# Optimization experiments

Measured on AMD Instinct MI355X. Metric: run time of the kernel, lower is better.

Reference implementation:

```python
import jax, jax.numpy as jnp
import numpy as np

N_NODES = 50000
N_EDGES = 400000
IN_DIM = 8
HIDDEN = 768
N_LAYERS = 4
LN_EPS = 1e-5


def setup_inputs() -> dict:
    key = jax.random.key(0)
    ks = jax.random.split(key, 10)
    x = jax.random.normal(ks[0], (N_NODES, IN_DIM), dtype=jnp.float32)
    edge_index = jax.random.randint(ks[1], (2, N_EDGES), 0, N_NODES, dtype=jnp.int32)
    # input projection
    s_in = 1.0 / np.sqrt(IN_DIM)
    Wp = jax.random.uniform(ks[2], (HIDDEN, IN_DIM), jnp.float32, -s_in, s_in)
    bp = jax.random.uniform(ks[3], (HIDDEN,), jnp.float32, -s_in, s_in)
    # stacked per-layer SAGEConv params (all layers have out_c == HIDDEN here)
    s_h = 1.0 / np.sqrt(HIDDEN)
    Wl = jax.random.uniform(ks[4], (N_LAYERS, HIDDEN, HIDDEN), jnp.float32, -s_h, s_h)  # lin_l (aggregated neighbors), has bias
    bl = jax.random.uniform(ks[5], (N_LAYERS, HIDDEN), jnp.float32, -s_h, s_h)
    Wr = jax.random.uniform(ks[6], (N_LAYERS, HIDDEN, HIDDEN), jnp.float32, -s_h, s_h)  # lin_r (root), no bias
    # LayerNorm params
    gamma = jnp.ones((N_LAYERS, HIDDEN), dtype=jnp.float32)
    beta = jnp.zeros((N_LAYERS, HIDDEN), dtype=jnp.float32)
    return {"x": x, "Wp": Wp, "bp": bp, "Wl": Wl, "bl": bl, "Wr": Wr,
            "gamma": gamma, "beta": beta, "edge_index": edge_index}


def _layer_norm(h, g, b):
    mu = jnp.mean(h, axis=-1, keepdims=True)
    var = jnp.mean(jnp.square(h - mu), axis=-1, keepdims=True)
    return (h - mu) * jax.lax.rsqrt(var + LN_EPS) * g + b


def reference(x, Wp, bp, Wl, bl, Wr, gamma, beta, edge_index):
    n = x.shape[0]
    src, dst = edge_index[0], edge_index[1]
    # in-degree per target node, clamped for mean
    deg = jax.ops.segment_sum(jnp.ones_like(dst, dtype=x.dtype), dst, num_segments=n)
    inv_deg = 1.0 / jnp.maximum(deg, 1.0)

    h = x @ Wp.T + bp  # [N, HIDDEN]

    def layer(h, params):
        Wl_i, bl_i, Wr_i, g_i, b_i = params
        # mean aggregation of source features at targets: [N, C]
        agg = jax.ops.segment_sum(h[src], dst, num_segments=n) * inv_deg[:, None]
        out = agg @ Wl_i.T + bl_i + h @ Wr_i.T  # SAGEConv
        out = _layer_norm(jax.nn.silu(out), g_i, b_i)  # norm(silu(conv))
        return out, None

    h, _ = jax.lax.scan(layer, h, (Wl, bl, Wr, gamma, beta))
    return h
```

## Files before the change

### kernel.cpp

```cpp
#include <hip/hip_runtime.h>

#define NN 50000
#define NE 400000
#define HID 768
#define NL 4

typedef short bf16x8_t __attribute__((ext_vector_type(8)));
typedef float f32x4_t __attribute__((ext_vector_type(4)));

__device__ __forceinline__ unsigned short f2bf(float f) {
  union { float f; unsigned int u; } c; c.f = f;
  unsigned int u = c.u;
  u += 0x7FFF + ((u >> 16) & 1);
  return (unsigned short)(u >> 16);
}
__device__ __forceinline__ float bf2f(unsigned short s) {
  union { unsigned int u; float f; } c; c.u = ((unsigned int)s) << 16;
  return c.f;
}

__device__ __forceinline__ void async16(const void* g, void* l) {
  __builtin_amdgcn_global_load_lds((const __attribute__((address_space(1))) void*)g,
                                   (__attribute__((address_space(3))) void*)l,
                                   16, 0, 0);
}

__global__ void k_zero2(int* __restrict__ a, int* __restrict__ b, int n) {
  int i = blockIdx.x * blockDim.x + threadIdx.x;
  if (i < n) { a[i] = 0; b[i] = 0; }
}

__global__ void k_cvt(const float* __restrict__ a, unsigned short* __restrict__ o, int n) {
  int i = blockIdx.x * blockDim.x + threadIdx.x;
  if (i < n) o[i] = f2bf(a[i]);
}

__global__ __launch_bounds__(256) void k_inproj(const float* __restrict__ x,
                                                const float* __restrict__ Wp,
                                                const float* __restrict__ bp,
                                                unsigned short* __restrict__ h) {
  int n = blockIdx.x;
  __shared__ float xs[8];
  if (threadIdx.x < 8) xs[threadIdx.x] = x[n * 8 + threadIdx.x];
  __syncthreads();
  for (int j = threadIdx.x; j < HID; j += 256) {
    const float* w = Wp + j * 8;
    float s = bp[j];
#pragma unroll
    for (int k = 0; k < 8; ++k) s += xs[k] * w[k];
    h[(size_t)n * HID + j] = f2bf(s);
  }
}

__global__ void k_deg(const int* __restrict__ dst, int* __restrict__ deg) {
  int i = blockIdx.x * blockDim.x + threadIdx.x;
  if (i < NE) atomicAdd(&deg[dst[i]], 1);
}

__global__ __launch_bounds__(1024) void k_scan(const int* __restrict__ deg, int* __restrict__ rowptr) {
  __shared__ int sm[1024];
  const int chunk = 49;
  int t = threadIdx.x;
  int start = t * chunk;
  int end = min(start + chunk, NN);
  int local = 0;
  for (int i = start; i < end; ++i) local += deg[i];
  sm[t] = local;
  __syncthreads();
  for (int off = 1; off < 1024; off <<= 1) {
    int v = (t >= off) ? sm[t - off] : 0;
    __syncthreads();
    sm[t] += v;
    __syncthreads();
  }
  int run = sm[t] - local;
  for (int i = start; i < end; ++i) { rowptr[i] = run; run += deg[i]; }
  if (start < NN && end == NN) rowptr[NN] = run;
}

__global__ void k_fill(const int* __restrict__ src, const int* __restrict__ dst,
                       const int* __restrict__ rowptr, int* __restrict__ cursor,
                       int* __restrict__ csr) {
  int i = blockIdx.x * blockDim.x + threadIdx.x;
  if (i < NE) {
    int d = dst[i];
    int pos = atomicAdd(&cursor[d], 1);
    csr[rowptr[d] + pos] = src[i];
  }
}

__global__ __launch_bounds__(192) void k_agg(const unsigned short* __restrict__ h,
                                             const int* __restrict__ csr,
                                             const int* __restrict__ rowptr,
                                             unsigned short* __restrict__ agg) {
  int n = blockIdx.x;
  int t = threadIdx.x;
  int beg = rowptr[n], end = rowptr[n + 1];
  float a0 = 0.f, a1 = 0.f, a2 = 0.f, a3 = 0.f;
  for (int i = beg; i < end; ++i) {
    int s = csr[i];
    ushort4 v = *(const ushort4*)(h + (size_t)s * HID + t * 4);
    a0 += bf2f(v.x); a1 += bf2f(v.y); a2 += bf2f(v.z); a3 += bf2f(v.w);
  }
  float inv = 1.0f / (float)max(end - beg, 1);
  ushort4 o;
  o.x = f2bf(a0 * inv); o.y = f2bf(a1 * inv); o.z = f2bf(a2 * inv); o.w = f2bf(a3 * inv);
  *(ushort4*)(agg + (size_t)n * HID + t * 4) = o;
}

#define BM 256
#define BN 256
#define NKT 48
#define GGRID 588

__global__ __launch_bounds__(512, 2) void k_gemm(const unsigned short* __restrict__ A0,
                                                 const unsigned short* __restrict__ A1,
                                                 const unsigned short* __restrict__ B0,
                                                 const unsigned short* __restrict__ B1,
                                                 const float* __restrict__ bias,
                                                 unsigned short* __restrict__ sact, int M) {
  __shared__ __align__(16) unsigned short As[4][BM * 32];
  __shared__ __align__(16) unsigned short Bs[4][BN * 32];

  int b = blockIdx.x;
  int xcd = b & 7;
  int j = b >> 3;
  int o = xcd * 73 + min(xcd, 4) + j;
  int band = o / 3;
  int nt3 = o - band * 3;
  int m0 = band * BM;
  int n0 = nt3 * BN;

  int tid = threadIdx.x;
  int lane = tid & 63;
  int w = tid >> 6;
  int wm = w >> 2, wn = w & 3;

  int rl = tid >> 2;
  int kgs = (tid & 3) ^ ((rl >> 1) & 3);
  size_t aO = (size_t)(m0 + rl) * HID + kgs * 8;
  size_t bO = (size_t)(n0 + rl) * HID + kgs * 8;
  const size_t hstep = (size_t)128 * HID;

  auto stageA = [&](int t) {
    const unsigned short* A = (t < 24) ? A0 : A1;
    size_t kk = (size_t)(t - ((t < 24) ? 0 : 24)) * 32;
    int s = t & 3;
    async16(A + aO + kk,         &As[s][w * 512]);
    async16(A + aO + hstep + kk, &As[s][4096 + w * 512]);
  };
  auto stageB = [&](int t) {
    const unsigned short* B = (t < 24) ? B0 : B1;
    size_t kk = (size_t)(t - ((t < 24) ? 0 : 24)) * 32;
    int s = t & 3;
    async16(B + bO + kk,         &Bs[s][w * 512]);
    async16(B + bO + hstep + kk, &Bs[s][4096 + w * 512]);
  };

  int mr = lane & 15, kq = lane >> 4;
  int sq = (kq ^ ((mr >> 1) & 3)) * 8;

  f32x4_t acc[8][4] = {};

  stageA(0); stageB(0); stageA(1); stageB(1); stageA(2);
  asm volatile("s_waitcnt vmcnt(6)" ::: "memory");
  __builtin_amdgcn_s_barrier();

  for (int t = 0; t < NKT; ++t) {
    int s = t & 3;
    bf16x8_t af[4], ag[4], bf[4];
#pragma unroll
    for (int i = 0; i < 4; ++i)
      af[i] = *(const bf16x8_t*)&As[s][(wm * 128 + i * 16 + mr) * 32 + sq];
#pragma unroll
    for (int i = 0; i < 4; ++i)
      bf[i] = *(const bf16x8_t*)&Bs[s][(wn * 64 + i * 16 + mr) * 32 + sq];
    if (t <= 45) stageB(t + 2);
    __builtin_amdgcn_s_barrier();
    asm volatile("s_waitcnt lgkmcnt(0)" ::: "memory");
    __builtin_amdgcn_sched_barrier(0);
    __builtin_amdgcn_s_setprio(1);
#pragma unroll
    for (int mt = 0; mt < 4; ++mt)
#pragma unroll
      for (int nt = 0; nt < 4; ++nt)
        acc[mt][nt] = __builtin_amdgcn_mfma_f32_16x16x32_bf16(af[mt], bf[nt], acc[mt][nt], 0, 0, 0);
    __builtin_amdgcn_s_setprio(0);
    __builtin_amdgcn_s_barrier();
#pragma unroll
    for (int i = 0; i < 4; ++i)
      ag[i] = *(const bf16x8_t*)&As[s][(wm * 128 + (i + 4) * 16 + mr) * 32 + sq];
    if (t <= 44) stageA(t + 3);
    __builtin_amdgcn_s_barrier();
    asm volatile("s_waitcnt lgkmcnt(0)" ::: "memory");
    __builtin_amdgcn_sched_barrier(0);
    __builtin_amdgcn_s_setprio(1);
#pragma unroll
    for (int mt = 0; mt < 4; ++mt)
#pragma unroll
      for (int nt = 0; nt < 4; ++nt)
        acc[mt + 4][nt] = __builtin_amdgcn_mfma_f32_16x16x32_bf16(ag[mt], bf[nt], acc[mt + 4][nt], 0, 0, 0);
    __builtin_amdgcn_s_setprio(0);
    if (t <= 44)      asm volatile("s_waitcnt vmcnt(6)" ::: "memory");
    else if (t == 45) asm volatile("s_waitcnt vmcnt(4)" ::: "memory");
    else if (t == 46) asm volatile("s_waitcnt vmcnt(0)" ::: "memory");
    __builtin_amdgcn_s_barrier();
  }

  int col = lane & 15;
  int rq = (lane >> 4) * 4;
#pragma unroll
  for (int mt = 0; mt < 8; ++mt) {
#pragma unroll
    for (int nt = 0; nt < 4; ++nt) {
      int jj = n0 + wn * 64 + nt * 16 + col;
      float bv = bias[jj];
#pragma unroll
      for (int r = 0; r < 4; ++r) {
        int gm = m0 + wm * 128 + mt * 16 + rq + r;
        if (gm < M) {
          float v = acc[mt][nt][r] + bv;
          float sv = v / (1.f + __expf(-v));
          sact[(size_t)gm * HID + jj] = f2bf(sv);
        }
      }
    }
  }
}

__global__ __launch_bounds__(256) void k_ln(const unsigned short* __restrict__ sact,
                                            const float* __restrict__ gamma,
                                            const float* __restrict__ beta,
                                            unsigned short* __restrict__ hout,
                                            float* __restrict__ fout) {
  int n = blockIdx.x;
  const unsigned short* p = sact + (size_t)n * HID;
  float v[3];
  float sum = 0.f, sq = 0.f;
#pragma unroll
  for (int i = 0; i < 3; ++i) {
    float s = bf2f(p[threadIdx.x + i * 256]);
    v[i] = s; sum += s; sq += s * s;
  }
#pragma unroll
  for (int off = 32; off >= 1; off >>= 1) {
    sum += __shfl_down(sum, off);
    sq  += __shfl_down(sq, off);
  }
  __shared__ float rs[4], rq2[4];
  int wv = threadIdx.x >> 6;
  if ((threadIdx.x & 63) == 0) { rs[wv] = sum; rq2[wv] = sq; }
  __syncthreads();
  if (threadIdx.x == 0) {
    float s = rs[0] + rs[1] + rs[2] + rs[3];
    float q = rq2[0] + rq2[1] + rq2[2] + rq2[3];
    rs[0] = s / (float)HID;
    rq2[0] = q / (float)HID;
  }
  __syncthreads();
  float mu = rs[0];
  float var = rq2[0] - mu * mu;
  float inv = rsqrtf(var + 1e-5f);
#pragma unroll
  for (int i = 0; i < 3; ++i) {
    int j = threadIdx.x + i * 256;
    float y = (v[i] - mu) * inv * gamma[j] + beta[j];
    if (fout) fout[(size_t)n * HID + j] = y;
    else      hout[(size_t)n * HID + j] = f2bf(y);
  }
}

extern "C" void kernel_launch(void* const* d_in, const int* in_sizes, int n_in,
                              void* d_out, int out_size, void* d_ws, size_t ws_size,
                              hipStream_t stream) {
  const float* x     = (const float*)d_in[0];
  const float* Wp    = (const float*)d_in[1];
  const float* bp    = (const float*)d_in[2];
  const float* Wl    = (const float*)d_in[3];
  const float* bl    = (const float*)d_in[4];
  const float* Wr    = (const float*)d_in[5];
  const float* gamma = (const float*)d_in[6];
  const float* beta  = (const float*)d_in[7];
  const int*   ei    = (const int*)d_in[8];
  float* out = (float*)d_out;

  const int* src = ei;
  const int* dst = ei + NE;

  char* p = (char*)d_ws;
  unsigned short* h    = (unsigned short*)p;              p += (size_t)NN * HID * 2;
  unsigned short* agg  = (unsigned short*)p;              p += (size_t)NN * HID * 2;
  unsigned short* sact = (unsigned short*)p;              p += (size_t)NN * HID * 2;
  unsigned short* Wlb  = (unsigned short*)p;              p += (size_t)NL * HID * HID * 2;
  unsigned short* Wrb  = (unsigned short*)p;              p += (size_t)NL * HID * HID * 2;
  int* deg             = (int*)p;                         p += (size_t)NN * 4;
  int* rowptr          = (int*)p;                         p += (size_t)(NN + 1) * 4 + 12;
  int* cursor          = (int*)p;                         p += (size_t)NN * 4;
  int* csr             = (int*)p;                         p += (size_t)NE * 4;

  k_zero2<<<(NN + 255) / 256, 256, 0, stream>>>(deg, cursor, NN);
  int wn = NL * HID * HID;
  k_cvt<<<(wn + 255) / 256, 256, 0, stream>>>(Wl, Wlb, wn);
  k_cvt<<<(wn + 255) / 256, 256, 0, stream>>>(Wr, Wrb, wn);
  k_inproj<<<NN, 256, 0, stream>>>(x, Wp, bp, h);
  k_deg<<<(NE + 255) / 256, 256, 0, stream>>>(dst, deg);
  k_scan<<<1, 1024, 0, stream>>>(deg, rowptr);
  k_fill<<<(NE + 255) / 256, 256, 0, stream>>>(src, dst, rowptr, cursor, csr);

  for (int l = 0; l < NL; ++l) {
    k_agg<<<NN, 192, 0, stream>>>(h, csr, rowptr, agg);
    k_gemm<<<GGRID, 512, 0, stream>>>(agg, h,
                                      Wlb + (size_t)l * HID * HID,
                                      Wrb + (size_t)l * HID * HID,
                                      bl + (size_t)l * HID, sact, NN);
    k_ln<<<NN, 256, 0, stream>>>(sact, gamma + (size_t)l * HID, beta + (size_t)l * HID,
                                 h, (l == NL - 1) ? out : nullptr);
  }
}
```

Before: 1.742 ms.

## Load A fragments directly to registers and halve GEMM N-tile to 128

The GEMM drops the LDS staging of the A operand. Each wave now loads its A fragments straight from global memory into registers through a three-deep register pipeline, while B is still staged asynchronously in LDS. The N tile shrinks from 256 to 128, which doubles the grid and remaps blocks to XCDs over six column tiles. The aim is to cut LDS traffic and barriers and to raise parallelism, at the cost of more register pressure, A rows re-read from global/L2 by every wave, and less reuse of each tile.

```diff
diff --git a/kernel.cpp b/kernel.cpp
--- a/kernel.cpp
+++ b/kernel.cpp
@@ -109,9 +109,9 @@
 }
 
 #define BM 256
-#define BN 256
+#define BN 128
 #define NKT 48
-#define GGRID 588
+#define GGRID 1176
 
 __global__ __launch_bounds__(512, 2) void k_gemm(const unsigned short* __restrict__ A0,
                                                  const unsigned short* __restrict__ A1,
@@ -119,109 +119,101 @@
                                                  const unsigned short* __restrict__ B1,
                                                  const float* __restrict__ bias,
                                                  unsigned short* __restrict__ sact, int M) {
-  __shared__ __align__(16) unsigned short As[4][BM * 32];
   __shared__ __align__(16) unsigned short Bs[4][BN * 32];
 
   int b = blockIdx.x;
-  int xcd = b & 7;
-  int j = b >> 3;
-  int o = xcd * 73 + min(xcd, 4) + j;
-  int band = o / 3;
-  int nt3 = o - band * 3;
-  int m0 = band * BM;
-  int n0 = nt3 * BN;
-
-  int tid = threadIdx.x;
-  int lane = tid & 63;
-  int w = tid >> 6;
+  int xcd = b & 7, jj = b >> 3;
+  int o = xcd * 147 + jj;
+  int band = o / 6, nt6 = o % 6;
+  int m0 = band * BM, n0 = nt6 * BN;
+
+  int tid = threadIdx.x, lane = tid & 63, w = tid >> 6;
   int wm = w >> 2, wn = w & 3;
 
   int rl = tid >> 2;
   int kgs = (tid & 3) ^ ((rl >> 1) & 3);
-  size_t aO = (size_t)(m0 + rl) * HID + kgs * 8;
-  size_t bO = (size_t)(n0 + rl) * HID + kgs * 8;
-  const size_t hstep = (size_t)128 * HID;
-
-  auto stageA = [&](int t) {
-    const unsigned short* A = (t < 24) ? A0 : A1;
-    size_t kk = (size_t)(t - ((t < 24) ? 0 : 24)) * 32;
+  size_t bsrc = (size_t)(n0 + rl) * (HID * 2) + kgs * 16;
+
+  int mr = lane & 15, kq = lane >> 4;
+  unsigned voffA[8];
+#pragma unroll
+  for (int i = 0; i < 8; ++i)
+    voffA[i] = (unsigned)(((wm * 128 + i * 16 + mr) * HID + kq * 8) * 2);
+
+  int sq = (kq ^ ((mr >> 1) & 3)) * 8;
+  int boffe[2];
+#pragma unroll
+  for (int nt = 0; nt < 2; ++nt)
+    boffe[nt] = (wn * 32 + nt * 16 + mr) * 32 + sq;
+
+  const char* Abase0 = (const char*)A0 + (size_t)m0 * (HID * 2);
+  const char* Abase1 = (const char*)A1 + (size_t)m0 * (HID * 2);
+
+  f32x4_t acc[8][2] = {};
+  bf16x8_t aS0[8], aS1[8], aS2[8];
+
+  auto loadA = [&](int tt, bf16x8_t (&af)[8]) {
+    const char* Ab = (tt < 24 ? Abase0 : Abase1) + (size_t)(tt < 24 ? tt : tt - 24) * 64;
+#pragma unroll
+    for (int i = 0; i < 8; ++i) af[i] = *(const bf16x8_t*)(Ab + voffA[i]);
+  };
+  auto stageB = [&](int tt) {
+    const char* Bb = (const char*)(tt < 24 ? B0 : B1) + (size_t)(tt < 24 ? tt : tt - 24) * 64;
+    async16(Bb + bsrc, &Bs[tt & 3][w * 512]);
+  };
+
+  auto body = [&](int t, bf16x8_t (&af)[8], int W) {
+    if (W == 18)      asm volatile("s_waitcnt vmcnt(18)" ::: "memory");
+    else if (W == 9)  asm volatile("s_waitcnt vmcnt(9)" ::: "memory");
+    else              asm volatile("s_waitcnt vmcnt(0)" ::: "memory");
+    __builtin_amdgcn_s_barrier();
     int s = t & 3;
-    async16(A + aO + kk,         &As[s][w * 512]);
-    async16(A + aO + hstep + kk, &As[s][4096 + w * 512]);
-  };
-  auto stageB = [&](int t) {
-    const unsigned short* B = (t < 24) ? B0 : B1;
-    size_t kk = (size_t)(t - ((t < 24) ? 0 : 24)) * 32;
-    int s = t & 3;
-    async16(B + bO + kk,         &Bs[s][w * 512]);
-    async16(B + bO + hstep + kk, &Bs[s][4096 + w * 512]);
-  };
-
-  int mr = lane & 15, kq = lane >> 4;
-  int sq = (kq ^ ((mr >> 1) & 3)) * 8;
-
-  f32x4_t acc[8][4] = {};
-
-  stageA(0); stageB(0); stageA(1); stageB(1); stageA(2);
-  asm volatile("s_waitcnt vmcnt(6)" ::: "memory");
-  __builtin_amdgcn_s_barrier();
-
-  for (int t = 0; t < NKT; ++t) {
-    int s = t & 3;
-    bf16x8_t af[4], ag[4], bf[4];
-#pragma unroll
-    for (int i = 0; i < 4; ++i)
-      af[i] = *(const bf16x8_t*)&As[s][(wm * 128 + i * 16 + mr) * 32 + sq];
-#pragma unroll
-    for (int i = 0; i < 4; ++i)
-      bf[i] = *(const bf16x8_t*)&Bs[s][(wn * 64 + i * 16 + mr) * 32 + sq];
-    if (t <= 45) stageB(t + 2);
-    __builtin_amdgcn_s_barrier();
+    bf16x8_t bf0 = *(const bf16x8_t*)&Bs[s][boffe[0]];
+    bf16x8_t bf1 = *(const bf16x8_t*)&Bs[s][boffe[1]];
     asm volatile("s_waitcnt lgkmcnt(0)" ::: "memory");
     __builtin_amdgcn_sched_barrier(0);
     __builtin_amdgcn_s_setprio(1);
 #pragma unroll
-    for (int mt = 0; mt < 4; ++mt)
-#pragma unroll
-      for (int nt = 0; nt < 4; ++nt)
-        acc[mt][nt] = __builtin_amdgcn_mfma_f32_16x16x32_bf16(af[mt], bf[nt], acc[mt][nt], 0, 0, 0);
+    for (int mt = 0; mt < 8; ++mt) {
+      acc[mt][0] = __builtin_amdgcn_mfma_f32_16x16x32_bf16(af[mt], bf0, acc[mt][0], 0, 0, 0);
+      acc[mt][1] = __builtin_amdgcn_mfma_f32_16x16x32_bf16(af[mt], bf1, acc[mt][1], 0, 0, 0);
+    }
     __builtin_amdgcn_s_setprio(0);
+    __builtin_amdgcn_sched_barrier(0);
+    int tt = t + 3;
+    if (tt < NKT) { loadA(tt, af); stageB(tt); }
+    __builtin_amdgcn_sched_barrier(0);
     __builtin_amdgcn_s_barrier();
-#pragma unroll
-    for (int i = 0; i < 4; ++i)
-      ag[i] = *(const bf16x8_t*)&As[s][(wm * 128 + (i + 4) * 16 + mr) * 32 + sq];
-    if (t <= 44) stageA(t + 3);
-    __builtin_amdgcn_s_barrier();
-    asm volatile("s_waitcnt lgkmcnt(0)" ::: "memory");
-    __builtin_amdgcn_sched_barrier(0);
-    __builtin_amdgcn_s_setprio(1);
-#pragma unroll
-    for (int mt = 0; mt < 4; ++mt)
-#pragma unroll
-      for (int nt = 0; nt < 4; ++nt)
-        acc[mt + 4][nt] = __builtin_amdgcn_mfma_f32_16x16x32_bf16(ag[mt], bf[nt], acc[mt + 4][nt], 0, 0, 0);
-    __builtin_amdgcn_s_setprio(0);
-    if (t <= 44)      asm volatile("s_waitcnt vmcnt(6)" ::: "memory");
-    else if (t == 45) asm volatile("s_waitcnt vmcnt(4)" ::: "memory");
-    else if (t == 46) asm volatile("s_waitcnt vmcnt(0)" ::: "memory");
-    __builtin_amdgcn_s_barrier();
-  }
+  };
+
+  loadA(0, aS0); stageB(0); __builtin_amdgcn_sched_barrier(0);
+  loadA(1, aS1); stageB(1); __builtin_amdgcn_sched_barrier(0);
+  loadA(2, aS2); stageB(2); __builtin_amdgcn_sched_barrier(0);
+
+  for (int t = 0; t < 45; t += 3) {
+    body(t,     aS0, 18);
+    body(t + 1, aS1, 18);
+    body(t + 2, aS2, 18);
+  }
+  body(45, aS0, 18);
+  body(46, aS1, 9);
+  body(47, aS2, 0);
 
   int col = lane & 15;
   int rq = (lane >> 4) * 4;
 #pragma unroll
   for (int mt = 0; mt < 8; ++mt) {
 #pragma unroll
-    for (int nt = 0; nt < 4; ++nt) {
-      int jj = n0 + wn * 64 + nt * 16 + col;
-      float bv = bias[jj];
+    for (int nt = 0; nt < 2; ++nt) {
+      int jc = n0 + wn * 32 + nt * 16 + col;
+      float bv = bias[jc];
 #pragma unroll
       for (int r = 0; r < 4; ++r) {
         int gm = m0 + wm * 128 + mt * 16 + rq + r;
         if (gm < M) {
           float v = acc[mt][nt][r] + bv;
           float sv = v / (1.f + __expf(-v));
-          sact[(size_t)gm * HID + jj] = f2bf(sv);
+          sact[(size_t)gm * HID + jc] = f2bf(sv);
         }
       }
     }
```

New measurement: 2.831 ms. 62.5% more time.
